# Optimization experiments

Measured on AMD Instinct MI355X. Metric: run time of the kernel, lower is better.

Reference implementation:

```python
import jax, jax.numpy as jnp
import numpy as np

D = 8           # spatial size of conv feature map
K = 24          # conv channels
Q = 128         # question embedding size
IN_SIZE = 2 * (K + 2) + Q  # 180
HID = 256
OUT = 28


def _coords(d):
    # faithful to torch float-tensor arithmetic: a/d is float division
    a = jnp.arange(d * d, dtype=jnp.float32)
    cx = (a / d - d / 2) / (d / 2.0)
    cy = (a % d - d / 2) / (d / 2.0)
    return jnp.stack([cx, cy], axis=1)  # [d^2, 2]


def setup_inputs() -> dict:
    key = jax.random.key(0)
    ks = jax.random.split(key, 16)
    s = 0.05
    inp = {
        "x": jax.random.normal(ks[0], (64, K, D, D), dtype=jnp.float32),
        "qst": jax.random.normal(ks[1], (64, Q), dtype=jnp.float32),
        # g MLP (weights stored [in, out])
        "g1_w": jax.random.normal(ks[2], (IN_SIZE, HID), dtype=jnp.float32) * s,
        "g1_b": jnp.zeros((HID,), dtype=jnp.float32),
        "g2_w": jax.random.normal(ks[3], (HID, HID), dtype=jnp.float32) * s,
        "g2_b": jnp.zeros((HID,), dtype=jnp.float32),
        "g3_w": jax.random.normal(ks[4], (HID, HID), dtype=jnp.float32) * s,
        "g3_b": jnp.zeros((HID,), dtype=jnp.float32),
        "g4_w": jax.random.normal(ks[5], (HID, HID), dtype=jnp.float32) * s,
        "g4_b": jnp.zeros((HID,), dtype=jnp.float32),
        # f MLP
        "f1_w": jax.random.normal(ks[6], (HID, HID), dtype=jnp.float32) * s,
        "f1_b": jnp.zeros((HID,), dtype=jnp.float32),
        "f2_w": jax.random.normal(ks[7], (HID, HID), dtype=jnp.float32) * s,
        "f2_b": jnp.zeros((HID,), dtype=jnp.float32),
        "f3_w": jax.random.normal(ks[8], (HID, OUT), dtype=jnp.float32) * s,
        "f3_b": jnp.zeros((OUT,), dtype=jnp.float32),
    }
    return inp


def _forward(x, qst, g1_w, g1_b, g2_w, g2_b, g3_w, g3_b, g4_w, g4_b,
             f1_w, f1_b, f2_w, f2_b, f3_w, f3_b):
    b, k, d, _ = x.shape
    n = d * d  # 64 objects
    # [b, n, k] object features + 2 coord channels -> [b, n, 26]
    xf = jnp.transpose(x.reshape(b, k, n), (0, 2, 1))
    ct = jnp.broadcast_to(_coords(d)[None], (b, n, 2))
    xf = jnp.concatenate([xf, ct], axis=2)                      # [b, n, 26]
    obj = k + 2
    # x_i: varies along axis 2 (original torch layout); x_j varies along axis 1 and carries qst
    xi = jnp.broadcast_to(xf[:, None, :, :], (b, n, n, obj))
    xjq = jnp.concatenate(
        [xf, jnp.broadcast_to(qst[:, None, :], (b, n, qst.shape[1]))], axis=2)
    xj = jnp.broadcast_to(xjq[:, :, None, :], (b, n, n, obj + qst.shape[1]))
    pair = jnp.concatenate([xi, xj], axis=3)                    # [b, n, n, 180]
    # g MLP over all pairs
    h = jax.nn.relu(pair @ g1_w + g1_b)
    h = jax.nn.relu(h @ g2_w + g2_b)
    h = jax.nn.relu(h @ g3_w + g3_b)
    h = jax.nn.relu(h @ g4_w + g4_b)                            # [b, n, n, 256]
    xg = jnp.sum(h, axis=(1, 2))                                # sum over d^4 pairs
    # f MLP (dropout is identity in eval mode)
    xf_ = jax.nn.relu(xg @ f1_w + f1_b)
    xf_ = jax.nn.relu(xf_ @ f2_w + f2_b)
    logits = xf_ @ f3_w + f3_b
    return jax.nn.log_softmax(logits, axis=-1)


def reference(x, qst, g1_w, g1_b, g2_w, g2_b, g3_w, g3_b, g4_w, g4_b,
              f1_w, f1_b, f2_w, f2_b, f3_w, f3_b):
    return _forward(x, qst, g1_w, g1_b, g2_w, g2_b, g3_w, g3_b, g4_w, g4_b,
                    f1_w, f1_b, f2_w, f2_b, f3_w, f3_b)
```

## Files before the change

kernel.cpp:

```cpp
#include <hip/hip_runtime.h>

typedef __bf16 bf16_t;
typedef __bf16 bf16x8 __attribute__((ext_vector_type(8)));
typedef __bf16 bf16x4 __attribute__((ext_vector_type(4)));
typedef float  f32x4  __attribute__((ext_vector_type(4)));


__device__ __forceinline__ int swz(int row, int col) {
  return (((col >> 3) ^ (row & 7)) << 3) | (col & 7);
}

__global__ __launch_bounds__(256) void rn_prep_kernel(
    const float* __restrict__ x, const float* __restrict__ qst,
    const float* __restrict__ g1w, const float* __restrict__ g1b,
    const float* __restrict__ g2w, const float* __restrict__ g3w,
    const float* __restrict__ g4w,
    float* __restrict__ A, float* __restrict__ C,
    bf16_t* __restrict__ Wt, float* __restrict__ xg)
{
  __shared__ float T[64][65];
  int blk = blockIdx.x;
  int n   = threadIdx.x;
  if (blk < 256) {
    int b  = blk >> 2;
    int jg = (blk & 3) * 16;
    float accQ = g1b[n];
    const float* qb = qst + b * 128;
    #pragma unroll 8
    for (int qi = 0; qi < 128; ++qi)
      accQ += qb[qi] * g1w[(52 + qi) * 256 + n];

    float w24 = g1w[24 * 256 + n], w25 = g1w[25 * 256 + n];
    float w50 = g1w[50 * 256 + n], w51 = g1w[51 * 256 + n];
    float accA[16], accC[16];
    #pragma unroll
    for (int t = 0; t < 16; ++t) {
      int j = jg + t;
      float cx = ((float)j * 0.125f - 4.0f) * 0.25f;
      float cy = ((float)(j & 7) - 4.0f) * 0.25f;
      accA[t] = cx * w24 + cy * w25;
      accC[t] = accQ + cx * w50 + cy * w51;
    }
    for (int c = 0; c < 24; ++c) {
      float wa = g1w[c * 256 + n];
      float wc = g1w[(26 + c) * 256 + n];
      const float* xc = x + (b * 24 + c) * 64 + jg;
      #pragma unroll
      for (int t = 0; t < 16; ++t) {
        float xv = xc[t];
        accA[t] += xv * wa;
        accC[t] += xv * wc;
      }
    }
    #pragma unroll
    for (int t = 0; t < 16; ++t) {
      A[(b * 64 + jg + t) * 256 + n] = accA[t];
      C[(b * 64 + jg + t) * 256 + n] = accC[t];
    }
  } else if (blk < 256 + 48) {
    int t   = blk - 256;
    int mat = t >> 4;
    int tl  = t & 15;
    int kt  = (tl & 3) * 64;
    int nt_ = (tl >> 2) * 64;
    const float* W = (mat == 0) ? g2w : (mat == 1 ? g3w : g4w);
    int lane = n & 63, w = n >> 6;
    #pragma unroll
    for (int it = 0; it < 16; ++it) {
      int kl = w * 16 + it;
      T[kl][lane] = W[(kt + kl) * 256 + nt_ + lane];
    }
    __syncthreads();
    #pragma unroll
    for (int it = 0; it < 16; ++it) {
      int nl = w * 16 + it;
      Wt[mat * 65536 + (nt_ + nl) * 256 + kt + lane] = (bf16_t)T[lane][nl];
    }
  } else {
    int idx = (blk - (256 + 48)) * 256 + n;
    xg[idx] = 0.f;
  }
}

__global__ __launch_bounds__(256, 2) void rn_main_kernel(
    const float* __restrict__ A, const float* __restrict__ C,
    const bf16_t* __restrict__ Wt,
    const float* __restrict__ g2b, const float* __restrict__ g3b,
    const float* __restrict__ g4b,
    float* __restrict__ xg)
{
  __shared__ bf16_t hbuf[128][256];

  int tid  = threadIdx.x;
  int bx   = blockIdx.x;
  int b    = bx >> 5;
  int ip   = bx & 31;
  int lane = tid & 63;
  int wave = tid >> 6;
  int n0   = wave * 64;

  {
    const float* Ab = A + (size_t)b * 64 * 256;
    const float* Cr = C + ((size_t)b * 64 + ip * 2) * 256;
    #pragma unroll
    for (int it = 0; it < 16; ++it) {
      int g = it * 256 + tid;
      int j = g >> 6;
      int n = (g & 63) * 4;
      const float4 a4 = *(const float4*)(Ab + j * 256 + n);
      const float4 c0 = *(const float4*)(Cr + n);
      const float4 c1 = *(const float4*)(Cr + 256 + n);
      bf16x4 v0, v1;
      v0[0] = (bf16_t)fmaxf(a4.x + c0.x, 0.f);
      v0[1] = (bf16_t)fmaxf(a4.y + c0.y, 0.f);
      v0[2] = (bf16_t)fmaxf(a4.z + c0.z, 0.f);
      v0[3] = (bf16_t)fmaxf(a4.w + c0.w, 0.f);
      v1[0] = (bf16_t)fmaxf(a4.x + c1.x, 0.f);
      v1[1] = (bf16_t)fmaxf(a4.y + c1.y, 0.f);
      v1[2] = (bf16_t)fmaxf(a4.z + c1.z, 0.f);
      v1[3] = (bf16_t)fmaxf(a4.w + c1.w, 0.f);
      *(bf16x4*)&hbuf[j][swz(j, n)] = v0;
      *(bf16x4*)&hbuf[64 + j][swz(64 + j, n)] = v1;
    }
  }

  const float* biases[3] = {g2b, g3b, g4b};
  int r = lane & 15;
  int q = lane >> 4;

  for (int L = 0; L < 3; ++L) {
    __syncthreads();
    const bf16_t* W = Wt + L * 65536;
    const float* bias = biases[L];

    f32x4 acc[4][8];
    #pragma unroll
    for (int nt = 0; nt < 4; ++nt)
      #pragma unroll
      for (int mt = 0; mt < 8; ++mt)
        #pragma unroll
        for (int e = 0; e < 4; ++e) acc[nt][mt][e] = 0.f;

    #pragma unroll
    for (int ks = 0; ks < 8; ++ks) {
      int k0 = ks * 32 + q * 8;
      bf16x8 wf[4], hf[8];
      #pragma unroll
      for (int nt = 0; nt < 4; ++nt)
        wf[nt] = *(const bf16x8*)&W[(n0 + nt * 16 + r) * 256 + k0];
      #pragma unroll
      for (int mt = 0; mt < 8; ++mt) {
        int row = mt * 16 + r;
        hf[mt] = *(const bf16x8*)&hbuf[row][swz(row, k0)];
      }
      #pragma unroll
      for (int nt = 0; nt < 4; ++nt)
        #pragma unroll
        for (int mt = 0; mt < 8; ++mt)
          acc[nt][mt] = __builtin_amdgcn_mfma_f32_16x16x32_bf16(
              wf[nt], hf[mt], acc[nt][mt], 0, 0, 0);
    }

    float4 bv[4];
    #pragma unroll
    for (int nt = 0; nt < 4; ++nt)
      bv[nt] = *(const float4*)&bias[n0 + nt * 16 + q * 4];

    if (L < 2) {
      __syncthreads();
      #pragma unroll
      for (int nt = 0; nt < 4; ++nt) {
        int col = n0 + nt * 16 + q * 4;
        #pragma unroll
        for (int mt = 0; mt < 8; ++mt) {
          int row = mt * 16 + r;
          bf16x4 v;
          v[0] = (bf16_t)fmaxf(acc[nt][mt][0] + bv[nt].x, 0.f);
          v[1] = (bf16_t)fmaxf(acc[nt][mt][1] + bv[nt].y, 0.f);
          v[2] = (bf16_t)fmaxf(acc[nt][mt][2] + bv[nt].z, 0.f);
          v[3] = (bf16_t)fmaxf(acc[nt][mt][3] + bv[nt].w, 0.f);
          *(bf16x4*)&hbuf[row][swz(row, col)] = v;
        }
      }
    } else {
      #pragma unroll
      for (int nt = 0; nt < 4; ++nt) {
        float p0 = 0.f, p1 = 0.f, p2 = 0.f, p3 = 0.f;
        #pragma unroll
        for (int mt = 0; mt < 8; ++mt) {
          p0 += fmaxf(acc[nt][mt][0] + bv[nt].x, 0.f);
          p1 += fmaxf(acc[nt][mt][1] + bv[nt].y, 0.f);
          p2 += fmaxf(acc[nt][mt][2] + bv[nt].z, 0.f);
          p3 += fmaxf(acc[nt][mt][3] + bv[nt].w, 0.f);
        }
        #pragma unroll
        for (int d = 1; d < 16; d <<= 1) {
          p0 += __shfl_xor(p0, d, 64);
          p1 += __shfl_xor(p1, d, 64);
          p2 += __shfl_xor(p2, d, 64);
          p3 += __shfl_xor(p3, d, 64);
        }
        if (r == 0) {
          int n = b * 256 + n0 + nt * 16 + q * 4;
          atomicAdd(&xg[n + 0], p0);
          atomicAdd(&xg[n + 1], p1);
          atomicAdd(&xg[n + 2], p2);
          atomicAdd(&xg[n + 3], p3);
        }
      }
    }
  }
}

__global__ __launch_bounds__(256) void rn_f_kernel(
    const float* __restrict__ xg,
    const float* __restrict__ f1w, const float* __restrict__ f1b,
    const float* __restrict__ f2w, const float* __restrict__ f2b,
    const float* __restrict__ f3w, const float* __restrict__ f3b,
    float* __restrict__ out)
{
  __shared__ float xs[256], t1[256], t2[256], lg[28], lse[1];
  int b = blockIdx.x, tid = threadIdx.x;
  xs[tid] = xg[b * 256 + tid];
  __syncthreads();
  float acc = f1b[tid];
  for (int k = 0; k < 256; ++k) acc += xs[k] * f1w[k * 256 + tid];
  t1[tid] = fmaxf(acc, 0.f);
  __syncthreads();
  acc = f2b[tid];
  for (int k = 0; k < 256; ++k) acc += t1[k] * f2w[k * 256 + tid];
  t2[tid] = fmaxf(acc, 0.f);
  __syncthreads();
  if (tid < 28) {
    float a2 = f3b[tid];
    for (int k = 0; k < 256; ++k) a2 += t2[k] * f3w[k * 28 + tid];
    lg[tid] = a2;
  }
  __syncthreads();
  if (tid == 0) {
    float m = lg[0];
    for (int j = 1; j < 28; ++j) m = fmaxf(m, lg[j]);
    float se = 0.f;
    for (int j = 0; j < 28; ++j) se += expf(lg[j] - m);
    lse[0] = m + logf(se);
  }
  __syncthreads();
  if (tid < 28) out[b * 28 + tid] = lg[tid] - lse[0];
}

extern "C" void kernel_launch(void* const* d_in, const int* in_sizes, int n_in,
                              void* d_out, int out_size, void* d_ws, size_t ws_size,
                              hipStream_t stream) {
  (void)in_sizes; (void)n_in; (void)out_size; (void)ws_size;
  const float* x   = (const float*)d_in[0];
  const float* qst = (const float*)d_in[1];
  const float* g1w = (const float*)d_in[2];
  const float* g1b = (const float*)d_in[3];
  const float* g2w = (const float*)d_in[4];
  const float* g2b = (const float*)d_in[5];
  const float* g3w = (const float*)d_in[6];
  const float* g3b = (const float*)d_in[7];
  const float* g4w = (const float*)d_in[8];
  const float* g4b = (const float*)d_in[9];
  const float* f1w = (const float*)d_in[10];
  const float* f1b = (const float*)d_in[11];
  const float* f2w = (const float*)d_in[12];
  const float* f2b = (const float*)d_in[13];
  const float* f3w = (const float*)d_in[14];
  const float* f3b = (const float*)d_in[15];
  float* out = (float*)d_out;

  float*  A  = (float*)d_ws;
  float*  C  = A + 4096 * 256;
  bf16_t* Wt = (bf16_t*)(C + 4096 * 256);
  float*  xg = (float*)((char*)Wt + 3 * 65536 * sizeof(bf16_t));

  rn_prep_kernel<<<256 + 48 + 64, 256, 0, stream>>>(
      x, qst, g1w, g1b, g2w, g3w, g4w, A, C, Wt, xg);
  rn_main_kernel<<<2048, 256, 0, stream>>>(A, C, Wt, g2b, g3b, g4b, xg);
  rn_f_kernel<<<64, 256, 0, stream>>>(xg, f1w, f1b, f2w, f2b, f3w, f3b, out);
}
```

Before: 254.1 us.

## Fuse f-MLP tail into main kernel via last-block counter and prefetch weights

Removes the separate f-MLP launch. Each main block increments a per-batch atomic counter after its atomic adds into xg, and the last of the 32 blocks for that batch runs the f-MLP and log-softmax, reusing the shared buffer. The weight fragments for the next k-step are also prefetched into registers, and the M loop is split into two halves to reduce live h fragments. The trade-offs are a fence and atomic per block, a serial tail on the last block, and higher register pressure from the double-buffered weights.

```diff
diff --git a/kernel.cpp b/kernel.cpp
--- a/kernel.cpp
+++ b/kernel.cpp
@@ -16,7 +16,7 @@
     const float* __restrict__ g2w, const float* __restrict__ g3w,
     const float* __restrict__ g4w,
     float* __restrict__ A, float* __restrict__ C,
-    bf16_t* __restrict__ Wt, float* __restrict__ xg)
+    bf16_t* __restrict__ Wt, float* __restrict__ xg, int* __restrict__ cnt)
 {
   __shared__ float T[64][65];
   int blk = blockIdx.x;
@@ -78,7 +78,8 @@
     }
   } else {
     int idx = (blk - (256 + 48)) * 256 + n;
-    xg[idx] = 0.f;
+    if (idx < 16384) xg[idx] = 0.f;
+    else if (idx < 16384 + 64) cnt[idx - 16384] = 0;
   }
 }
 
@@ -87,9 +88,14 @@
     const bf16_t* __restrict__ Wt,
     const float* __restrict__ g2b, const float* __restrict__ g3b,
     const float* __restrict__ g4b,
-    float* __restrict__ xg)
+    float* __restrict__ xg, int* __restrict__ cnt,
+    const float* __restrict__ f1w, const float* __restrict__ f1b,
+    const float* __restrict__ f2w, const float* __restrict__ f2b,
+    const float* __restrict__ f3w, const float* __restrict__ f3b,
+    float* __restrict__ out)
 {
   __shared__ bf16_t hbuf[128][256];
+  __shared__ int s_dof;
 
   int tid  = threadIdx.x;
   int bx   = blockIdx.x;
@@ -124,14 +130,13 @@
     }
   }
 
-  const float* biases[3] = {g2b, g3b, g4b};
   int r = lane & 15;
   int q = lane >> 4;
 
   for (int L = 0; L < 3; ++L) {
     __syncthreads();
-    const bf16_t* W = Wt + L * 65536;
-    const float* bias = biases[L];
+    const bf16_t* Wr = Wt + L * 65536 + (n0 + r) * 256;
+    const float* bias = (L == 0) ? g2b : (L == 1 ? g3b : g4b);
 
     f32x4 acc[4][8];
     #pragma unroll
@@ -140,25 +145,37 @@
       for (int mt = 0; mt < 8; ++mt)
         #pragma unroll
         for (int e = 0; e < 4; ++e) acc[nt][mt][e] = 0.f;
+
+    bf16x8 wf_cur[4], wf_nxt[4];
+    #pragma unroll
+    for (int nt = 0; nt < 4; ++nt)
+      wf_cur[nt] = *(const bf16x8*)&Wr[nt * 4096 + q * 8];
 
     #pragma unroll
     for (int ks = 0; ks < 8; ++ks) {
       int k0 = ks * 32 + q * 8;
-      bf16x8 wf[4], hf[8];
-      #pragma unroll
-      for (int nt = 0; nt < 4; ++nt)
-        wf[nt] = *(const bf16x8*)&W[(n0 + nt * 16 + r) * 256 + k0];
-      #pragma unroll
-      for (int mt = 0; mt < 8; ++mt) {
-        int row = mt * 16 + r;
-        hf[mt] = *(const bf16x8*)&hbuf[row][swz(row, k0)];
+      if (ks < 7) {
+        #pragma unroll
+        for (int nt = 0; nt < 4; ++nt)
+          wf_nxt[nt] = *(const bf16x8*)&Wr[nt * 4096 + k0 + 32];
       }
       #pragma unroll
-      for (int nt = 0; nt < 4; ++nt)
-        #pragma unroll
-        for (int mt = 0; mt < 8; ++mt)
-          acc[nt][mt] = __builtin_amdgcn_mfma_f32_16x16x32_bf16(
-              wf[nt], hf[mt], acc[nt][mt], 0, 0, 0);
+      for (int mh = 0; mh < 2; ++mh) {
+        bf16x8 hf[4];
+        #pragma unroll
+        for (int mt = 0; mt < 4; ++mt) {
+          int row = mh * 64 + mt * 16 + r;
+          hf[mt] = *(const bf16x8*)&hbuf[row][swz(row, k0)];
+        }
+        #pragma unroll
+        for (int nt = 0; nt < 4; ++nt)
+          #pragma unroll
+          for (int mt = 0; mt < 4; ++mt)
+            acc[nt][mh * 4 + mt] = __builtin_amdgcn_mfma_f32_16x16x32_bf16(
+                wf_cur[nt], hf[mt], acc[nt][mh * 4 + mt], 0, 0, 0);
+      }
+      #pragma unroll
+      for (int nt = 0; nt < 4; ++nt) wf_cur[nt] = wf_nxt[nt];
     }
 
     float4 bv[4];
@@ -169,19 +186,22 @@
     if (L < 2) {
       __syncthreads();
       #pragma unroll
-      for (int nt = 0; nt < 4; ++nt) {
-        int col = n0 + nt * 16 + q * 4;
-        #pragma unroll
-        for (int mt = 0; mt < 8; ++mt) {
-          int row = mt * 16 + r;
-          bf16x4 v;
-          v[0] = (bf16_t)fmaxf(acc[nt][mt][0] + bv[nt].x, 0.f);
-          v[1] = (bf16_t)fmaxf(acc[nt][mt][1] + bv[nt].y, 0.f);
-          v[2] = (bf16_t)fmaxf(acc[nt][mt][2] + bv[nt].z, 0.f);
-          v[3] = (bf16_t)fmaxf(acc[nt][mt][3] + bv[nt].w, 0.f);
-          *(bf16x4*)&hbuf[row][swz(row, col)] = v;
-        }
-      }
+      for (int mh = 0; mh < 2; ++mh)
+        #pragma unroll
+        for (int nt = 0; nt < 4; ++nt) {
+          int col = n0 + nt * 16 + q * 4;
+          #pragma unroll
+          for (int mt = 0; mt < 4; ++mt) {
+            int row = mh * 64 + mt * 16 + r;
+            f32x4 a = acc[nt][mh * 4 + mt];
+            bf16x4 v;
+            v[0] = (bf16_t)fmaxf(a[0] + bv[nt].x, 0.f);
+            v[1] = (bf16_t)fmaxf(a[1] + bv[nt].y, 0.f);
+            v[2] = (bf16_t)fmaxf(a[2] + bv[nt].z, 0.f);
+            v[3] = (bf16_t)fmaxf(a[3] + bv[nt].w, 0.f);
+            *(bf16x4*)&hbuf[row][swz(row, col)] = v;
+          }
+        }
     } else {
       #pragma unroll
       for (int nt = 0; nt < 4; ++nt) {
@@ -210,42 +230,48 @@
       }
     }
   }
-}
-
-__global__ __launch_bounds__(256) void rn_f_kernel(
-    const float* __restrict__ xg,
-    const float* __restrict__ f1w, const float* __restrict__ f1b,
-    const float* __restrict__ f2w, const float* __restrict__ f2b,
-    const float* __restrict__ f3w, const float* __restrict__ f3b,
-    float* __restrict__ out)
-{
-  __shared__ float xs[256], t1[256], t2[256], lg[28], lse[1];
-  int b = blockIdx.x, tid = threadIdx.x;
-  xs[tid] = xg[b * 256 + tid];
-  __syncthreads();
-  float acc = f1b[tid];
-  for (int k = 0; k < 256; ++k) acc += xs[k] * f1w[k * 256 + tid];
-  t1[tid] = fmaxf(acc, 0.f);
-  __syncthreads();
-  acc = f2b[tid];
-  for (int k = 0; k < 256; ++k) acc += t1[k] * f2w[k * 256 + tid];
-  t2[tid] = fmaxf(acc, 0.f);
-  __syncthreads();
-  if (tid < 28) {
-    float a2 = f3b[tid];
-    for (int k = 0; k < 256; ++k) a2 += t2[k] * f3w[k * 28 + tid];
-    lg[tid] = a2;
-  }
+
   __syncthreads();
   if (tid == 0) {
-    float m = lg[0];
-    for (int j = 1; j < 28; ++j) m = fmaxf(m, lg[j]);
-    float se = 0.f;
-    for (int j = 0; j < 28; ++j) se += expf(lg[j] - m);
-    lse[0] = m + logf(se);
+    __threadfence();
+    int old = __hip_atomic_fetch_add(&cnt[b], 1, __ATOMIC_ACQ_REL,
+                                     __HIP_MEMORY_SCOPE_AGENT);
+    s_dof = (old == 31);
   }
   __syncthreads();
-  if (tid < 28) out[b * 28 + tid] = lg[tid] - lse[0];
+  if (s_dof) {
+    float* xs = (float*)&hbuf[0][0];
+    float* t1 = xs + 256;
+    float* t2 = t1 + 256;
+    float* lg = t2 + 256;
+    float* ls = lg + 28;
+    xs[tid] = __hip_atomic_load(&xg[b * 256 + tid], __ATOMIC_RELAXED,
+                                __HIP_MEMORY_SCOPE_AGENT);
+    __syncthreads();
+    float acc1 = f1b[tid];
+    for (int k = 0; k < 256; ++k) acc1 += xs[k] * f1w[k * 256 + tid];
+    t1[tid] = fmaxf(acc1, 0.f);
+    __syncthreads();
+    float acc2 = f2b[tid];
+    for (int k = 0; k < 256; ++k) acc2 += t1[k] * f2w[k * 256 + tid];
+    t2[tid] = fmaxf(acc2, 0.f);
+    __syncthreads();
+    if (tid < 28) {
+      float a2 = f3b[tid];
+      for (int k = 0; k < 256; ++k) a2 += t2[k] * f3w[k * 28 + tid];
+      lg[tid] = a2;
+    }
+    __syncthreads();
+    if (tid == 0) {
+      float m = lg[0];
+      for (int j = 1; j < 28; ++j) m = fmaxf(m, lg[j]);
+      float se = 0.f;
+      for (int j = 0; j < 28; ++j) se += expf(lg[j] - m);
+      ls[0] = m + logf(se);
+    }
+    __syncthreads();
+    if (tid < 28) out[b * 28 + tid] = lg[tid] - ls[0];
+  }
 }
 
 extern "C" void kernel_launch(void* const* d_in, const int* in_sizes, int n_in,
@@ -274,9 +300,11 @@
   float*  C  = A + 4096 * 256;
   bf16_t* Wt = (bf16_t*)(C + 4096 * 256);
   float*  xg = (float*)((char*)Wt + 3 * 65536 * sizeof(bf16_t));
-
-  rn_prep_kernel<<<256 + 48 + 64, 256, 0, stream>>>(
-      x, qst, g1w, g1b, g2w, g3w, g4w, A, C, Wt, xg);
-  rn_main_kernel<<<2048, 256, 0, stream>>>(A, C, Wt, g2b, g3b, g4b, xg);
-  rn_f_kernel<<<64, 256, 0, stream>>>(xg, f1w, f1b, f2w, f2b, f3w, f3b, out);
+  int*    cnt = (int*)(xg + 64 * 256);
+
+  rn_prep_kernel<<<256 + 48 + 65, 256, 0, stream>>>(
+      x, qst, g1w, g1b, g2w, g3w, g4w, A, C, Wt, xg, cnt);
+  rn_main_kernel<<<2048, 256, 0, stream>>>(
+      A, C, Wt, g2b, g3b, g4b, xg, cnt,
+      f1w, f1b, f2w, f2b, f3w, f3b, out);
 }
```

Result: slower. 312.5 us (+23.0%).
